# Kernel tuning notes

Measured on AMD Instinct MI355X. Metric: run time of the kernel, lower is better.

## Reference

```python
import jax, jax.numpy as jnp
import numpy as np

N, DIM, L = 65536, 128, 8


def setup_inputs() -> dict:
    rng = np.random.default_rng(0)
    # depth-consistent random tree: node 0 is root (depth 0); every other node
    # gets depth in [1, L-1] and a parent chosen uniformly among depth-1 nodes.
    depth = np.zeros(N, dtype=np.int64)
    depth[1:] = rng.integers(1, L, size=N - 1)
    depth = np.sort(depth)  # node 0 stays root; contiguous levels
    parent = np.full(N, N, dtype=np.int64)  # sentinel N for the root (dropped in segment_sum slice)
    for d in range(1, L):
        cur = np.nonzero(depth == d)[0]
        prev = np.nonzero(depth == d - 1)[0]
        parent[cur] = rng.choice(prev, size=cur.size)
    key = jax.random.key(0)
    k = jax.random.split(key, 5)
    s = 1.0 / np.sqrt(DIM)
    return {
        "x": jax.random.normal(k[0], (N, DIM), jnp.float32),
        "parent": jnp.asarray(parent),
        "depth": jnp.asarray(depth),
        "Wioux": jax.random.normal(k[1], (DIM, 3 * DIM), jnp.float32) * s,
        "Wiouh": jax.random.normal(k[2], (DIM, 3 * DIM), jnp.float32) * s,
        "Wfx": jax.random.normal(k[3], (DIM, DIM), jnp.float32) * s,
        "Wfh": jax.random.normal(k[4], (DIM, DIM), jnp.float32) * s,
        "n_levels": L,
    }


def reference(x, parent, depth, Wioux, Wiouh, Wfx, Wfh, n_levels):
    n, dim = x.shape
    xi = x @ Wioux          # [N, 3d]  precomputed input projections
    xf = x @ Wfx            # [N, d]
    pidx = jnp.minimum(parent, n - 1)  # safe gather index (root sentinel clipped; root is never a child)
    h = jnp.zeros_like(x)
    c = jnp.zeros_like(x)
    # process tree bottom-up, one depth level at a time (equivalent to the
    # torch depth-descending per-node loop since children are exactly one level deeper)
    for d in range(int(n_levels) - 1, -1, -1):
        child = depth == d + 1          # nodes that are children of level-d nodes
        cm = child[:, None]
        h_sum = jax.ops.segment_sum(jnp.where(cm, h, 0.0), parent, num_segments=n + 1)[:n]
        n_child = jax.ops.segment_sum(child.astype(x.dtype), parent, num_segments=n + 1)[:n]
        # per-child forget gate: sigmoid(fx(x[parent]) + fh(h_child))
        f = jax.nn.sigmoid(xf[pidx] + h @ Wfh)
        fc_sum = jax.ops.segment_sum(jnp.where(cm, f * c, 0.0), parent, num_segments=n + 1)[:n]
        i_, o_, u_ = jnp.split(xi + h_sum @ Wiouh, 3, axis=-1)
        c_int = fc_sum + jax.nn.sigmoid(i_) * jnp.tanh(u_)
        h_int = jax.nn.sigmoid(o_) * jnp.tanh(c_int)
        leaf = (n_child == 0)[:, None]  # leaves: h = x, c = tanh(x) (as in torch code)
        h_new = jnp.where(leaf, x, h_int)
        c_new = jnp.where(leaf, jnp.tanh(x), c_int)
        lvl = (depth == d)[:, None]
        h = jnp.where(lvl, h_new, h)
        c = jnp.where(lvl, c_new, c)
    return h
```

## Files before the change

kernel.cpp:

```cpp
#include <hip/hip_runtime.h>
#include <hip/hip_bf16.h>

#define DIM 128
#define LVL 8

typedef unsigned int u32;
typedef unsigned short u16;

using bf16x8 = __attribute__((ext_vector_type(8))) short;
using f32x4  = __attribute__((ext_vector_type(4))) float;

__device__ __forceinline__ float bf2f(u16 u) { union { u32 i; float f; } v; v.i = ((u32)u) << 16; return v.f; }
__device__ __forceinline__ u16 f2bf(float f) { __hip_bfloat16 b = __float2bfloat16(f); return *reinterpret_cast<u16*>(&b); }
__device__ __forceinline__ u32 pk2(float lo, float hi) { return (u32)f2bf(lo) | ((u32)f2bf(hi) << 16); }
__device__ __forceinline__ float sigf(float x) { return 1.f / (1.f + __expf(-x)); }
__device__ __forceinline__ float tanhfast(float x) { return 1.f - 2.f / (__expf(2.f * x) + 1.f); }

__global__ void k_levels(const int* __restrict__ depth, int n, int* __restrict__ ofs) {
  int d = threadIdx.x;
  if (d > LVL) return;
  int lo = 0, hi = n;
  while (lo < hi) { int mid = (lo + hi) >> 1; if (depth[mid] < d) lo = mid + 1; else hi = mid; }
  ofs[d] = lo;
}

__global__ void k_mark(const int* __restrict__ parent, int n, int* __restrict__ haschild) {
  int j = blockIdx.x * blockDim.x + threadIdx.x;
  if (j >= n) return;
  int p = parent[j];
  if (p >= 0 && p < n) haschild[p] = 1;
}

__global__ void k_prep(const float* __restrict__ Wioux, const float* __restrict__ Wiouh,
                       const float* __restrict__ Wfx, const float* __restrict__ Wfh,
                       u16* __restrict__ WcT, u16* __restrict__ WhT, u16* __restrict__ WfhT) {
  int i = blockIdx.x * 256 + threadIdx.x;
  if (i >= 1024 * 128) return;
  int c = i >> 7, k = i & 127;
  float v; u16* dst;
  if (c < 512) {
    v = (c < 384) ? Wioux[(size_t)k * 384 + c] : Wfx[(size_t)k * 128 + (c - 384)];
    dst = &WcT[(size_t)c * 128 + k];
  } else if (c < 896) {
    int cc = c - 512; v = Wiouh[(size_t)k * 384 + cc]; dst = &WhT[(size_t)cc * 128 + k];
  } else {
    int cc = c - 896; v = Wfh[(size_t)k * 128 + cc]; dst = &WfhT[(size_t)cc * 128 + k];
  }
  *dst = f2bf(v);
}

__global__ __launch_bounds__(256) void k_big(const float* __restrict__ x, const u16* __restrict__ WcT,
                                             const int* __restrict__ haschild, u16* __restrict__ xi, int n) {
  __shared__ __align__(16) char smem[16384 + 32768];
  char* xsb = smem;
  char* wtb = smem + 16384;
  u16* dbuf = (u16*)(smem + 16384);
  __shared__ int s_any;
  int tid = threadIdx.x;
  int wave = tid >> 6, lane = tid & 63, m = lane & 15, kg = lane >> 4;
  int row0 = blockIdx.x * 64;
  if (tid == 0) {
    int a = 0;
    for (int r = 0; r < 64 && row0 + r < n; ++r) a |= haschild[row0 + r];
    s_any = a;
  }
  __syncthreads();
  if (!s_any) return;
  for (int i = tid; i < 64 * 16; i += 256) {
    int r = i >> 4, c8 = (i & 15) * 8;
    int gr = row0 + r;
    uint4 o = make_uint4(0u, 0u, 0u, 0u);
    if (gr < n) {
      float4 a = *(const float4*)(x + (size_t)gr * DIM + c8);
      float4 b = *(const float4*)(x + (size_t)gr * DIM + c8 + 4);
      o = make_uint4(pk2(a.x, a.y), pk2(a.z, a.w), pk2(b.x, b.y), pk2(b.z, b.w));
    }
    *(uint4*)(xsb + r * 256 + ((c8 * 2) ^ ((r & 7) << 4))) = o;
  }
  int arow = wave * 16 + m;
  for (int ci = 0; ci < 4; ++ci) {
    __syncthreads();
    for (int i = tid; i < 128 * 16; i += 256) {
      int cl = i >> 4, k8 = (i & 15) * 8;
      uint4 v = *(const uint4*)(WcT + (size_t)(ci * 128 + cl) * 128 + k8);
      *(uint4*)(wtb + cl * 256 + ((k8 * 2) ^ ((cl & 7) << 4))) = v;
    }
    __syncthreads();
    f32x4 acc[8];
    #pragma unroll
    for (int nt = 0; nt < 8; ++nt) acc[nt] = (f32x4){0.f, 0.f, 0.f, 0.f};
    #pragma unroll
    for (int kk = 0; kk < 4; ++kk) {
      int kbyte = kk * 64 + kg * 16;
      bf16x8 a = *(const bf16x8*)(xsb + arow * 256 + (kbyte ^ ((arow & 7) << 4)));
      #pragma unroll
      for (int nt = 0; nt < 8; ++nt) {
        int col = nt * 16 + m;
        bf16x8 b = *(const bf16x8*)(wtb + col * 256 + (kbyte ^ ((col & 7) << 4)));
        acc[nt] = __builtin_amdgcn_mfma_f32_16x16x32_bf16(a, b, acc[nt], 0, 0, 0);
      }
    }
    __syncthreads();
    #pragma unroll
    for (int nt = 0; nt < 8; ++nt)
      #pragma unroll
      for (int r = 0; r < 4; ++r)
        dbuf[(wave * 16 + kg * 4 + r) * 136 + nt * 16 + m] = f2bf(acc[nt][r]);
    __syncthreads();
    int r2 = tid >> 2, q = tid & 3;
    int gr = row0 + r2;
    if (gr < n && haschild[gr]) {
      const u16* src = dbuf + r2 * 136 + q * 32;
      u16* dst = xi + (size_t)gr * 512 + ci * 128 + q * 32;
      #pragma unroll
      for (int seg = 0; seg < 4; ++seg)
        *(uint4*)(dst + seg * 8) = *(const uint4*)(src + seg * 8);
    }
  }
}

__global__ __launch_bounds__(256) void k_child(const float* __restrict__ h, const float* __restrict__ cbuf,
    const u16* __restrict__ xi, const u16* __restrict__ WfhT, const int* __restrict__ parent,
    const int* __restrict__ ofs, float* __restrict__ hsum, float* __restrict__ fcsum, int d) {
  __shared__ __align__(16) char smem[16384 + 33792];
  char* hsb = smem;
  char* wtb = smem + 16384;
  float* dbuf = (float*)(smem + 16384);
  __shared__ int ps[64];
  __shared__ int s_uni;
  int c0 = ofs[d + 1], c1 = ofs[d + 2];
  int tid = threadIdx.x;
  int wave = tid >> 6, lane = tid & 63, m = lane & 15, kg = lane >> 4;
  int arow = wave * 16 + m;
  for (int row0 = c0 + (int)blockIdx.x * 64; row0 < c1; row0 += (int)gridDim.x * 64) {
    int nrows = min(64, c1 - row0);
    if (tid < 64) ps[tid] = (tid < nrows) ? parent[row0 + tid] : -1;
    for (int i = tid; i < 64 * 16; i += 256) {
      int r = i >> 4, c8 = (i & 15) * 8;
      uint4 o = make_uint4(0u, 0u, 0u, 0u);
      if (r < nrows) {
        const float* hp = h + (size_t)(row0 + r) * DIM + c8;
        float4 a = *(const float4*)hp; float4 b = *(const float4*)(hp + 4);
        o = make_uint4(pk2(a.x, a.y), pk2(a.z, a.w), pk2(b.x, b.y), pk2(b.z, b.w));
      }
      *(uint4*)(hsb + r * 256 + ((c8 * 2) ^ ((r & 7) << 4))) = o;
    }
    __syncthreads();
    if (tid == 0) {
      int u = 1, p0 = ps[0];
      for (int r = 1; r < nrows; ++r) if (ps[r] != p0) { u = 0; break; }
      s_uni = u;
    }
    for (int i = tid; i < 128 * 16; i += 256) {
      int cl = i >> 4, k8 = (i & 15) * 8;
      uint4 v = *(const uint4*)(WfhT + (size_t)cl * 128 + k8);
      *(uint4*)(wtb + cl * 256 + ((k8 * 2) ^ ((cl & 7) << 4))) = v;
    }
    __syncthreads();
    f32x4 acc[8];
    #pragma unroll
    for (int nt = 0; nt < 8; ++nt) acc[nt] = (f32x4){0.f, 0.f, 0.f, 0.f};
    #pragma unroll
    for (int kk = 0; kk < 4; ++kk) {
      int kbyte = kk * 64 + kg * 16;
      bf16x8 a = *(const bf16x8*)(hsb + arow * 256 + (kbyte ^ ((arow & 7) << 4)));
      #pragma unroll
      for (int nt = 0; nt < 8; ++nt) {
        int col = nt * 16 + m;
        bf16x8 b = *(const bf16x8*)(wtb + col * 256 + (kbyte ^ ((col & 7) << 4)));
        acc[nt] = __builtin_amdgcn_mfma_f32_16x16x32_bf16(a, b, acc[nt], 0, 0, 0);
      }
    }
    __syncthreads();
    if (s_uni) {
      int p = ps[0];
      #pragma unroll
      for (int nt = 0; nt < 8; ++nt) {
        int col = nt * 16 + m;
        #pragma unroll
        for (int r = 0; r < 4; ++r) {
          int rl = wave * 16 + kg * 4 + r;
          float fc = 0.f;
          if (rl < nrows) {
            float xfv = bf2f(xi[(size_t)p * 512 + 384 + col]);
            float cv = cbuf[(size_t)(row0 + rl) * DIM + col];
            fc = sigf(xfv + acc[nt][r]) * cv;
          }
          dbuf[rl * 132 + col] = fc;
        }
      }
      __syncthreads();
      if (tid < 128) {
        float sh = 0.f, sf = 0.f;
        for (int r = 0; r < 64; ++r) {
          u16 hv = *(const u16*)(hsb + r * 256 + ((2 * tid) ^ ((r & 7) << 4)));
          sh += bf2f(hv);
          sf += dbuf[r * 132 + tid];
        }
        atomicAdd(&hsum[(size_t)p * DIM + tid], sh);
        atomicAdd(&fcsum[(size_t)p * DIM + tid], sf);
      }
      __syncthreads();
    } else {
      #pragma unroll
      for (int nt = 0; nt < 8; ++nt) {
        int col = nt * 16 + m;
        #pragma unroll
        for (int r = 0; r < 4; ++r) {
          int rl = wave * 16 + kg * 4 + r;
          if (rl < nrows) {
            int p = ps[rl];
            float xfv = bf2f(xi[(size_t)p * 512 + 384 + col]);
            float cv = cbuf[(size_t)(row0 + rl) * DIM + col];
            float fc = sigf(xfv + acc[nt][r]) * cv;
            atomicAdd(&fcsum[(size_t)p * DIM + col], fc);
            u16 hv = *(const u16*)(hsb + rl * 256 + ((2 * col) ^ ((rl & 7) << 4)));
            atomicAdd(&hsum[(size_t)p * DIM + col], bf2f(hv));
          }
        }
      }
      __syncthreads();
    }
  }
}

__global__ __launch_bounds__(256) void k_node(const float* __restrict__ x, const u16* __restrict__ WhT,
    const u16* __restrict__ xi, const float* __restrict__ hsum, const float* __restrict__ fcsum,
    const int* __restrict__ haschild, const int* __restrict__ ofs,
    float* __restrict__ h, float* __restrict__ cbuf, int d) {
  __shared__ __align__(16) char smem[16384 + 32768];
  char* hsb = smem;
  char* wtb = smem + 16384;
  __shared__ int flags[64];
  __shared__ int s_any;
  int v0 = ofs[d], v1 = ofs[d + 1];
  int tid = threadIdx.x;
  int wave = tid >> 6, lane = tid & 63, m = lane & 15, kg = lane >> 4;
  int arow = wave * 16 + m;
  for (int row0 = v0 + (int)blockIdx.x * 64; row0 < v1; row0 += (int)gridDim.x * 64) {
    int nrows = min(64, v1 - row0);
    if (tid < 64) flags[tid] = (tid < nrows) ? haschild[row0 + tid] : 0;
    __syncthreads();
    if (tid == 0) { int a = 0; for (int r = 0; r < 64; ++r) a |= flags[r]; s_any = a; }
    __syncthreads();
    if (!s_any) {
      for (int i = tid; i < nrows * 32; i += 256) {
        int r = i >> 5, c4 = (i & 31) * 4;
        int gr = row0 + r;
        float4 xv = *(const float4*)(x + (size_t)gr * DIM + c4);
        float4 cv = make_float4(tanhfast(xv.x), tanhfast(xv.y), tanhfast(xv.z), tanhfast(xv.w));
        *(float4*)(h + (size_t)gr * DIM + c4) = xv;
        *(float4*)(cbuf + (size_t)gr * DIM + c4) = cv;
      }
      __syncthreads();
      continue;
    }
    for (int i = tid; i < 64 * 16; i += 256) {
      int r = i >> 4, c8 = (i & 15) * 8;
      int gr = row0 + r;
      uint4 o = make_uint4(0u, 0u, 0u, 0u);
      if (r < nrows) {
        float4 a = *(const float4*)(hsum + (size_t)gr * DIM + c8);
        float4 b = *(const float4*)(hsum + (size_t)gr * DIM + c8 + 4);
        o = make_uint4(pk2(a.x, a.y), pk2(a.z, a.w), pk2(b.x, b.y), pk2(b.z, b.w));
      }
      *(uint4*)(hsb + r * 256 + ((c8 * 2) ^ ((r & 7) << 4))) = o;
    }
    f32x4 acc[3][8];
    #pragma unroll
    for (int ci = 0; ci < 3; ++ci)
      #pragma unroll
      for (int nt = 0; nt < 8; ++nt) acc[ci][nt] = (f32x4){0.f, 0.f, 0.f, 0.f};
    for (int ci = 0; ci < 3; ++ci) {
      __syncthreads();
      for (int i = tid; i < 128 * 16; i += 256) {
        int cl = i >> 4, k8 = (i & 15) * 8;
        uint4 v = *(const uint4*)(WhT + (size_t)(ci * 128 + cl) * 128 + k8);
        *(uint4*)(wtb + cl * 256 + ((k8 * 2) ^ ((cl & 7) << 4))) = v;
      }
      __syncthreads();
      #pragma unroll
      for (int kk = 0; kk < 4; ++kk) {
        int kbyte = kk * 64 + kg * 16;
        bf16x8 a = *(const bf16x8*)(hsb + arow * 256 + (kbyte ^ ((arow & 7) << 4)));
        #pragma unroll
        for (int nt = 0; nt < 8; ++nt) {
          int col = nt * 16 + m;
          bf16x8 b = *(const bf16x8*)(wtb + col * 256 + (kbyte ^ ((col & 7) << 4)));
          acc[ci][nt] = __builtin_amdgcn_mfma_f32_16x16x32_bf16(a, b, acc[ci][nt], 0, 0, 0);
        }
      }
    }
    #pragma unroll
    for (int nt = 0; nt < 8; ++nt) {
      int col = nt * 16 + m;
      #pragma unroll
      for (int r = 0; r < 4; ++r) {
        int rl = wave * 16 + kg * 4 + r;
        int grow = row0 + rl;
        if (rl >= nrows) continue;
        bool leaf = (flags[rl] == 0);
        float iv = bf2f(xi[(size_t)grow * 512 + col])       + acc[0][nt][r];
        float ov = bf2f(xi[(size_t)grow * 512 + 128 + col]) + acc[1][nt][r];
        float uv = bf2f(xi[(size_t)grow * 512 + 256 + col]) + acc[2][nt][r];
        float fcv = fcsum[(size_t)grow * DIM + col];
        float xv = x[(size_t)grow * DIM + col];
        float ci_ = fcv + sigf(iv) * tanhfast(uv);
        float hv = leaf ? xv : sigf(ov) * tanhfast(ci_);
        float cv = leaf ? tanhfast(xv) : ci_;
        h[(size_t)grow * DIM + col] = hv;
        cbuf[(size_t)grow * DIM + col] = cv;
      }
    }
    __syncthreads();
  }
}

extern "C" void kernel_launch(void* const* d_in, const int* in_sizes, int n_in,
                              void* d_out, int out_size, void* d_ws, size_t ws_size,
                              hipStream_t stream) {
  const float* x    = (const float*)d_in[0];
  const int* parent = (const int*)d_in[1];
  const int* depth  = (const int*)d_in[2];
  const float* Wioux = (const float*)d_in[3];
  const float* Wiouh = (const float*)d_in[4];
  const float* Wfx   = (const float*)d_in[5];
  const float* Wfh   = (const float*)d_in[6];
  int n = in_sizes[0] / DIM;
  float* h = (float*)d_out;

  u16*   WcT  = (u16*)d_ws;
  u16*   WhT  = WcT + 512 * 128;
  u16*   WfhT = WhT + 384 * 128;
  u16*   xi   = WfhT + 128 * 128;
  float* cbuf = (float*)(xi + (size_t)n * 512);
  float* hsum = cbuf + (size_t)n * DIM;
  float* fcsum = hsum + (size_t)n * DIM;
  int*   haschild = (int*)(fcsum + (size_t)n * DIM);
  int*   ofs  = haschild + n;

  hipMemsetAsync(hsum, 0, (size_t)2 * n * DIM * sizeof(float) + (size_t)n * sizeof(int), stream);
  k_prep<<<512, 256, 0, stream>>>(Wioux, Wiouh, Wfx, Wfh, WcT, WhT, WfhT);
  k_levels<<<1, 32, 0, stream>>>(depth, n, ofs);
  k_mark<<<(n + 255) / 256, 256, 0, stream>>>(parent, n, haschild);
  k_big<<<(n + 63) / 64, 256, 0, stream>>>(x, WcT, haschild, xi, n);

  for (int d = LVL - 1; d >= 0; --d) {
    if (d < LVL - 1)
      k_child<<<160, 256, 0, stream>>>(h, cbuf, xi, WfhT, parent, ofs, hsum, fcsum, d);
    k_node<<<160, 256, 0, stream>>>(x, WhT, xi, hsum, fcsum, haschild, ofs, h, cbuf, d);
  }
}
```

Before: 405.5 us.

## Fuse per-level node and child kernels, keep cell state in registers

```diff
diff --git a/kernel.cpp b/kernel.cpp
--- a/kernel.cpp
+++ b/kernel.cpp
@@ -78,14 +78,28 @@
     *(uint4*)(xsb + r * 256 + ((c8 * 2) ^ ((r & 7) << 4))) = o;
   }
   int arow = wave * 16 + m;
+  uint4 wreg[8];
+  #pragma unroll
+  for (int j = 0; j < 8; ++j) {
+    int i = tid + j * 256;
+    wreg[j] = *(const uint4*)(WcT + (size_t)(i >> 4) * 128 + (i & 15) * 8);
+  }
   for (int ci = 0; ci < 4; ++ci) {
     __syncthreads();
-    for (int i = tid; i < 128 * 16; i += 256) {
+    #pragma unroll
+    for (int j = 0; j < 8; ++j) {
+      int i = tid + j * 256;
       int cl = i >> 4, k8 = (i & 15) * 8;
-      uint4 v = *(const uint4*)(WcT + (size_t)(ci * 128 + cl) * 128 + k8);
-      *(uint4*)(wtb + cl * 256 + ((k8 * 2) ^ ((cl & 7) << 4))) = v;
-    }
-    __syncthreads();
+      *(uint4*)(wtb + cl * 256 + ((k8 * 2) ^ ((cl & 7) << 4))) = wreg[j];
+    }
+    __syncthreads();
+    if (ci < 3) {
+      #pragma unroll
+      for (int j = 0; j < 8; ++j) {
+        int i = tid + j * 256;
+        wreg[j] = *(const uint4*)(WcT + (size_t)((ci + 1) * 128 + (i >> 4)) * 128 + (i & 15) * 8);
+      }
+    }
     f32x4 acc[8];
     #pragma unroll
     for (int nt = 0; nt < 8; ++nt) acc[nt] = (f32x4){0.f, 0.f, 0.f, 0.f};
@@ -119,166 +133,110 @@
   }
 }
 
-__global__ __launch_bounds__(256) void k_child(const float* __restrict__ h, const float* __restrict__ cbuf,
-    const u16* __restrict__ xi, const u16* __restrict__ WfhT, const int* __restrict__ parent,
-    const int* __restrict__ ofs, float* __restrict__ hsum, float* __restrict__ fcsum, int d) {
+__global__ __launch_bounds__(256) void k_level(const float* __restrict__ x,
+    const u16* __restrict__ WhT, const u16* __restrict__ WfhT, const u16* __restrict__ xi,
+    const int* __restrict__ haschild, const int* __restrict__ parent,
+    const int* __restrict__ ofs, float* __restrict__ hout,
+    float* hsum, float* fcsum, int d) {
   __shared__ __align__(16) char smem[16384 + 33792];
   char* hsb = smem;
   char* wtb = smem + 16384;
   float* dbuf = (float*)(smem + 16384);
   __shared__ int ps[64];
-  __shared__ int s_uni;
-  int c0 = ofs[d + 1], c1 = ofs[d + 2];
-  int tid = threadIdx.x;
-  int wave = tid >> 6, lane = tid & 63, m = lane & 15, kg = lane >> 4;
-  int arow = wave * 16 + m;
-  for (int row0 = c0 + (int)blockIdx.x * 64; row0 < c1; row0 += (int)gridDim.x * 64) {
-    int nrows = min(64, c1 - row0);
-    if (tid < 64) ps[tid] = (tid < nrows) ? parent[row0 + tid] : -1;
-    for (int i = tid; i < 64 * 16; i += 256) {
-      int r = i >> 4, c8 = (i & 15) * 8;
-      uint4 o = make_uint4(0u, 0u, 0u, 0u);
-      if (r < nrows) {
-        const float* hp = h + (size_t)(row0 + r) * DIM + c8;
-        float4 a = *(const float4*)hp; float4 b = *(const float4*)(hp + 4);
-        o = make_uint4(pk2(a.x, a.y), pk2(a.z, a.w), pk2(b.x, b.y), pk2(b.z, b.w));
-      }
-      *(uint4*)(hsb + r * 256 + ((c8 * 2) ^ ((r & 7) << 4))) = o;
-    }
-    __syncthreads();
-    if (tid == 0) {
-      int u = 1, p0 = ps[0];
-      for (int r = 1; r < nrows; ++r) if (ps[r] != p0) { u = 0; break; }
-      s_uni = u;
-    }
-    for (int i = tid; i < 128 * 16; i += 256) {
-      int cl = i >> 4, k8 = (i & 15) * 8;
-      uint4 v = *(const uint4*)(WfhT + (size_t)cl * 128 + k8);
-      *(uint4*)(wtb + cl * 256 + ((k8 * 2) ^ ((cl & 7) << 4))) = v;
-    }
-    __syncthreads();
-    f32x4 acc[8];
-    #pragma unroll
-    for (int nt = 0; nt < 8; ++nt) acc[nt] = (f32x4){0.f, 0.f, 0.f, 0.f};
-    #pragma unroll
-    for (int kk = 0; kk < 4; ++kk) {
-      int kbyte = kk * 64 + kg * 16;
-      bf16x8 a = *(const bf16x8*)(hsb + arow * 256 + (kbyte ^ ((arow & 7) << 4)));
-      #pragma unroll
-      for (int nt = 0; nt < 8; ++nt) {
-        int col = nt * 16 + m;
-        bf16x8 b = *(const bf16x8*)(wtb + col * 256 + (kbyte ^ ((col & 7) << 4)));
-        acc[nt] = __builtin_amdgcn_mfma_f32_16x16x32_bf16(a, b, acc[nt], 0, 0, 0);
-      }
-    }
-    __syncthreads();
-    if (s_uni) {
-      int p = ps[0];
-      #pragma unroll
-      for (int nt = 0; nt < 8; ++nt) {
-        int col = nt * 16 + m;
-        #pragma unroll
-        for (int r = 0; r < 4; ++r) {
-          int rl = wave * 16 + kg * 4 + r;
-          float fc = 0.f;
-          if (rl < nrows) {
-            float xfv = bf2f(xi[(size_t)p * 512 + 384 + col]);
-            float cv = cbuf[(size_t)(row0 + rl) * DIM + col];
-            fc = sigf(xfv + acc[nt][r]) * cv;
-          }
-          dbuf[rl * 132 + col] = fc;
-        }
-      }
-      __syncthreads();
-      if (tid < 128) {
-        float sh = 0.f, sf = 0.f;
-        for (int r = 0; r < 64; ++r) {
-          u16 hv = *(const u16*)(hsb + r * 256 + ((2 * tid) ^ ((r & 7) << 4)));
-          sh += bf2f(hv);
-          sf += dbuf[r * 132 + tid];
-        }
-        atomicAdd(&hsum[(size_t)p * DIM + tid], sh);
-        atomicAdd(&fcsum[(size_t)p * DIM + tid], sf);
-      }
-      __syncthreads();
-    } else {
-      #pragma unroll
-      for (int nt = 0; nt < 8; ++nt) {
-        int col = nt * 16 + m;
-        #pragma unroll
-        for (int r = 0; r < 4; ++r) {
-          int rl = wave * 16 + kg * 4 + r;
-          if (rl < nrows) {
-            int p = ps[rl];
-            float xfv = bf2f(xi[(size_t)p * 512 + 384 + col]);
-            float cv = cbuf[(size_t)(row0 + rl) * DIM + col];
-            float fc = sigf(xfv + acc[nt][r]) * cv;
-            atomicAdd(&fcsum[(size_t)p * DIM + col], fc);
-            u16 hv = *(const u16*)(hsb + rl * 256 + ((2 * col) ^ ((rl & 7) << 4)));
-            atomicAdd(&hsum[(size_t)p * DIM + col], bf2f(hv));
-          }
-        }
-      }
-      __syncthreads();
-    }
-  }
-}
-
-__global__ __launch_bounds__(256) void k_node(const float* __restrict__ x, const u16* __restrict__ WhT,
-    const u16* __restrict__ xi, const float* __restrict__ hsum, const float* __restrict__ fcsum,
-    const int* __restrict__ haschild, const int* __restrict__ ofs,
-    float* __restrict__ h, float* __restrict__ cbuf, int d) {
-  __shared__ __align__(16) char smem[16384 + 32768];
-  char* hsb = smem;
-  char* wtb = smem + 16384;
   __shared__ int flags[64];
-  __shared__ int s_any;
+  __shared__ int s_uni, s_anyp;
   int v0 = ofs[d], v1 = ofs[d + 1];
   int tid = threadIdx.x;
   int wave = tid >> 6, lane = tid & 63, m = lane & 15, kg = lane >> 4;
   int arow = wave * 16 + m;
   for (int row0 = v0 + (int)blockIdx.x * 64; row0 < v1; row0 += (int)gridDim.x * 64) {
     int nrows = min(64, v1 - row0);
-    if (tid < 64) flags[tid] = (tid < nrows) ? haschild[row0 + tid] : 0;
-    __syncthreads();
-    if (tid == 0) { int a = 0; for (int r = 0; r < 64; ++r) a |= flags[r]; s_any = a; }
-    __syncthreads();
-    if (!s_any) {
-      for (int i = tid; i < nrows * 32; i += 256) {
-        int r = i >> 5, c4 = (i & 31) * 4;
-        int gr = row0 + r;
-        float4 xv = *(const float4*)(x + (size_t)gr * DIM + c4);
-        float4 cv = make_float4(tanhfast(xv.x), tanhfast(xv.y), tanhfast(xv.z), tanhfast(xv.w));
-        *(float4*)(h + (size_t)gr * DIM + c4) = xv;
-        *(float4*)(cbuf + (size_t)gr * DIM + c4) = cv;
-      }
-      __syncthreads();
-      continue;
-    }
-    for (int i = tid; i < 64 * 16; i += 256) {
-      int r = i >> 4, c8 = (i & 15) * 8;
-      int gr = row0 + r;
-      uint4 o = make_uint4(0u, 0u, 0u, 0u);
-      if (r < nrows) {
-        float4 a = *(const float4*)(hsum + (size_t)gr * DIM + c8);
-        float4 b = *(const float4*)(hsum + (size_t)gr * DIM + c8 + 4);
-        o = make_uint4(pk2(a.x, a.y), pk2(a.z, a.w), pk2(b.x, b.y), pk2(b.z, b.w));
-      }
-      *(uint4*)(hsb + r * 256 + ((c8 * 2) ^ ((r & 7) << 4))) = o;
-    }
+    if (tid < 64) {
+      flags[tid] = (tid < nrows) ? haschild[row0 + tid] : 0;
+      ps[tid] = (tid < nrows) ? parent[row0 + tid] : -1;
+    }
+    __syncthreads();
+    if (tid == 0) {
+      int a = 0; for (int r = 0; r < 64; ++r) a |= flags[r];
+      s_anyp = a;
+      int u = 1, p0 = ps[0];
+      for (int r = 1; r < nrows; ++r) if (ps[r] != p0) { u = 0; break; }
+      s_uni = u;
+    }
+    __syncthreads();
     f32x4 acc[3][8];
     #pragma unroll
     for (int ci = 0; ci < 3; ++ci)
       #pragma unroll
       for (int nt = 0; nt < 8; ++nt) acc[ci][nt] = (f32x4){0.f, 0.f, 0.f, 0.f};
-    for (int ci = 0; ci < 3; ++ci) {
-      __syncthreads();
+    if (s_anyp) {
+      for (int i = tid; i < 64 * 16; i += 256) {
+        int r = i >> 4, c8 = (i & 15) * 8;
+        uint4 o = make_uint4(0u, 0u, 0u, 0u);
+        if (r < nrows) {
+          const float* hp = hsum + (size_t)(row0 + r) * DIM + c8;
+          float4 a = *(const float4*)hp; float4 b = *(const float4*)(hp + 4);
+          o = make_uint4(pk2(a.x, a.y), pk2(a.z, a.w), pk2(b.x, b.y), pk2(b.z, b.w));
+        }
+        *(uint4*)(hsb + r * 256 + ((c8 * 2) ^ ((r & 7) << 4))) = o;
+      }
+      #pragma unroll
+      for (int ci = 0; ci < 3; ++ci) {
+        for (int i = tid; i < 128 * 16; i += 256) {
+          int cl = i >> 4, k8 = (i & 15) * 8;
+          uint4 v = *(const uint4*)(WhT + (size_t)(ci * 128 + cl) * 128 + k8);
+          *(uint4*)(wtb + cl * 256 + ((k8 * 2) ^ ((cl & 7) << 4))) = v;
+        }
+        __syncthreads();
+        #pragma unroll
+        for (int kk = 0; kk < 4; ++kk) {
+          int kbyte = kk * 64 + kg * 16;
+          bf16x8 a = *(const bf16x8*)(hsb + arow * 256 + (kbyte ^ ((arow & 7) << 4)));
+          #pragma unroll
+          for (int nt = 0; nt < 8; ++nt) {
+            int col = nt * 16 + m;
+            bf16x8 b = *(const bf16x8*)(wtb + col * 256 + (kbyte ^ ((col & 7) << 4)));
+            acc[ci][nt] = __builtin_amdgcn_mfma_f32_16x16x32_bf16(a, b, acc[ci][nt], 0, 0, 0);
+          }
+        }
+        __syncthreads();
+      }
+    }
+    float cc[8][4];
+    #pragma unroll
+    for (int nt = 0; nt < 8; ++nt) {
+      int col = nt * 16 + m;
+      #pragma unroll
+      for (int r = 0; r < 4; ++r) {
+        int rl = wave * 16 + kg * 4 + r;
+        int grow = row0 + rl;
+        float hv = 0.f, cv = 0.f;
+        if (rl < nrows) {
+          bool leaf = (flags[rl] == 0);
+          float xv = x[(size_t)grow * DIM + col];
+          float iv = bf2f(xi[(size_t)grow * 512 + col])       + acc[0][nt][r];
+          float ov = bf2f(xi[(size_t)grow * 512 + 128 + col]) + acc[1][nt][r];
+          float uv = bf2f(xi[(size_t)grow * 512 + 256 + col]) + acc[2][nt][r];
+          float fcv = fcsum[(size_t)grow * DIM + col];
+          float ci_ = fcv + sigf(iv) * tanhfast(uv);
+          hv = leaf ? xv : sigf(ov) * tanhfast(ci_);
+          cv = leaf ? tanhfast(xv) : ci_;
+          hout[(size_t)grow * DIM + col] = hv;
+        }
+        cc[nt][r] = cv;
+        if (d > 0) *(u16*)(hsb + rl * 256 + ((2 * col) ^ ((rl & 7) << 4))) = f2bf(hv);
+      }
+    }
+    if (d > 0) {
       for (int i = tid; i < 128 * 16; i += 256) {
         int cl = i >> 4, k8 = (i & 15) * 8;
-        uint4 v = *(const uint4*)(WhT + (size_t)(ci * 128 + cl) * 128 + k8);
+        uint4 v = *(const uint4*)(WfhT + (size_t)cl * 128 + k8);
         *(uint4*)(wtb + cl * 256 + ((k8 * 2) ^ ((cl & 7) << 4))) = v;
       }
       __syncthreads();
+      f32x4 fp[8];
+      #pragma unroll
+      for (int nt = 0; nt < 8; ++nt) fp[nt] = (f32x4){0.f, 0.f, 0.f, 0.f};
       #pragma unroll
       for (int kk = 0; kk < 4; ++kk) {
         int kbyte = kk * 64 + kg * 16;
@@ -287,32 +245,56 @@
         for (int nt = 0; nt < 8; ++nt) {
           int col = nt * 16 + m;
           bf16x8 b = *(const bf16x8*)(wtb + col * 256 + (kbyte ^ ((col & 7) << 4)));
-          acc[ci][nt] = __builtin_amdgcn_mfma_f32_16x16x32_bf16(a, b, acc[ci][nt], 0, 0, 0);
-        }
-      }
-    }
-    #pragma unroll
-    for (int nt = 0; nt < 8; ++nt) {
-      int col = nt * 16 + m;
-      #pragma unroll
-      for (int r = 0; r < 4; ++r) {
-        int rl = wave * 16 + kg * 4 + r;
-        int grow = row0 + rl;
-        if (rl >= nrows) continue;
-        bool leaf = (flags[rl] == 0);
-        float iv = bf2f(xi[(size_t)grow * 512 + col])       + acc[0][nt][r];
-        float ov = bf2f(xi[(size_t)grow * 512 + 128 + col]) + acc[1][nt][r];
-        float uv = bf2f(xi[(size_t)grow * 512 + 256 + col]) + acc[2][nt][r];
-        float fcv = fcsum[(size_t)grow * DIM + col];
-        float xv = x[(size_t)grow * DIM + col];
-        float ci_ = fcv + sigf(iv) * tanhfast(uv);
-        float hv = leaf ? xv : sigf(ov) * tanhfast(ci_);
-        float cv = leaf ? tanhfast(xv) : ci_;
-        h[(size_t)grow * DIM + col] = hv;
-        cbuf[(size_t)grow * DIM + col] = cv;
-      }
-    }
-    __syncthreads();
+          fp[nt] = __builtin_amdgcn_mfma_f32_16x16x32_bf16(a, b, fp[nt], 0, 0, 0);
+        }
+      }
+      __syncthreads();
+      if (s_uni) {
+        int p = ps[0];
+        #pragma unroll
+        for (int nt = 0; nt < 8; ++nt) {
+          int col = nt * 16 + m;
+          float xfv = bf2f(xi[(size_t)p * 512 + 384 + col]);
+          #pragma unroll
+          for (int r = 0; r < 4; ++r) {
+            int rl = wave * 16 + kg * 4 + r;
+            float fc = (rl < nrows) ? sigf(xfv + fp[nt][r]) * cc[nt][r] : 0.f;
+            dbuf[rl * 132 + col] = fc;
+          }
+        }
+        __syncthreads();
+        if (tid < 128) {
+          float sh = 0.f, sf = 0.f;
+          for (int r = 0; r < 64; ++r) {
+            sh += bf2f(*(const u16*)(hsb + r * 256 + ((2 * tid) ^ ((r & 7) << 4))));
+            sf += dbuf[r * 132 + tid];
+          }
+          atomicAdd(&hsum[(size_t)p * DIM + tid], sh);
+          atomicAdd(&fcsum[(size_t)p * DIM + tid], sf);
+        }
+        __syncthreads();
+      } else {
+        #pragma unroll
+        for (int nt = 0; nt < 8; ++nt) {
+          int col = nt * 16 + m;
+          #pragma unroll
+          for (int r = 0; r < 4; ++r) {
+            int rl = wave * 16 + kg * 4 + r;
+            if (rl < nrows) {
+              int p = ps[rl];
+              float xfv = bf2f(xi[(size_t)p * 512 + 384 + col]);
+              float fc = sigf(xfv + fp[nt][r]) * cc[nt][r];
+              atomicAdd(&fcsum[(size_t)p * DIM + col], fc);
+              float hvv = bf2f(*(const u16*)(hsb + rl * 256 + ((2 * col) ^ ((rl & 7) << 4))));
+              atomicAdd(&hsum[(size_t)p * DIM + col], hvv);
+            }
+          }
+        }
+        __syncthreads();
+      }
+    } else {
+      __syncthreads();
+    }
   }
 }
 
@@ -333,8 +315,7 @@
   u16*   WhT  = WcT + 512 * 128;
   u16*   WfhT = WhT + 384 * 128;
   u16*   xi   = WfhT + 128 * 128;
-  float* cbuf = (float*)(xi + (size_t)n * 512);
-  float* hsum = cbuf + (size_t)n * DIM;
+  float* hsum = (float*)(xi + (size_t)n * 512);
   float* fcsum = hsum + (size_t)n * DIM;
   int*   haschild = (int*)(fcsum + (size_t)n * DIM);
   int*   ofs  = haschild + n;
@@ -345,9 +326,6 @@
   k_mark<<<(n + 255) / 256, 256, 0, stream>>>(parent, n, haschild);
   k_big<<<(n + 63) / 64, 256, 0, stream>>>(x, WcT, haschild, xi, n);
 
-  for (int d = LVL - 1; d >= 0; --d) {
-    if (d < LVL - 1)
-      k_child<<<160, 256, 0, stream>>>(h, cbuf, xi, WfhT, parent, ofs, hsum, fcsum, d);
-    k_node<<<160, 256, 0, stream>>>(x, WhT, xi, hsum, fcsum, haschild, ofs, h, cbuf, d);
-  }
-}
+  for (int d = LVL - 1; d >= 0; --d)
+    k_level<<<256, 256, 0, stream>>>(x, WhT, WfhT, xi, haschild, parent, ofs, h, hsum, fcsum, d);
+}
```

New measurement: 389.9 us. 3.9% less time.
